# Kernel optimization log

Hardware: AMD Instinct MI355X
Metric: run time of the kernel (lower is better)

## Reference

```python
import jax, jax.numpy as jnp
import numpy as np

B_SZ, L, D_MODEL = 2, 1024, 1024
D_INNER, D_STATE, D_CONV = 2048, 16, 4
EPS = 1e-6


def setup_inputs() -> dict:
    key = jax.random.key(0)
    ks = jax.random.split(key, 8)
    def n(k, shape, scale=0.02):
        return jax.random.normal(k, shape, jnp.float32) * scale
    return {
        "x": jax.random.normal(ks[0], (B_SZ, L, D_MODEL), jnp.float32),
        "W_in": n(ks[1], (D_MODEL, 2 * D_INNER)),
        "b_in": jnp.zeros((2 * D_INNER,), jnp.float32),
        "conv_w": n(ks[2], (D_INNER, 1, D_CONV), 0.2),
        "conv_b": jnp.zeros((D_INNER,), jnp.float32),
        "W_xp": n(ks[3], (D_INNER, 2 * D_STATE)),
        "b_xp": jnp.zeros((2 * D_STATE,), jnp.float32),
        "W_dt": n(ks[4], (D_INNER, D_INNER)),
        "b_dt": jnp.full((D_INNER,), -1.0, jnp.float32),
        # torch code does log(randn) (NaN-prone); use log of positive uniform instead
        "A_log": jnp.log(jax.random.uniform(ks[5], (D_INNER, D_STATE), jnp.float32, 0.5, 1.5)),
        "D_skip": jnp.ones((D_INNER,), jnp.float32),
        "W_out": n(ks[6], (D_INNER, D_MODEL)),
        "b_out": jnp.zeros((D_MODEL,), jnp.float32),
        "alpha": jnp.ones((D_MODEL,), jnp.float32),
        "beta": jnp.zeros((D_MODEL,), jnp.float32),
    }


def _selective_scan(xc, delta, A, Bm, Cm, D_skip):
    # xc, delta: (B,L,di); A: (di,ds); Bm, Cm: (B,L,ds)
    dA = jnp.exp(delta[..., None] * A)                     # (B,L,di,ds)
    dBx = (delta * xc)[..., None] * Bm[:, :, None, :]      # (B,L,di,ds)
    h0 = jnp.zeros((xc.shape[0], xc.shape[2], A.shape[1]), xc.dtype)

    def step(h, inp):
        dA_t, dBx_t, C_t = inp
        h = dA_t * h + dBx_t                               # (B,di,ds)
        y_t = jnp.einsum('bds,bs->bd', h, C_t)
        return h, y_t

    _, ys = jax.lax.scan(
        step, h0,
        (dA.transpose(1, 0, 2, 3), dBx.transpose(1, 0, 2, 3), Cm.transpose(1, 0, 2)))
    y = ys.transpose(1, 0, 2)                              # (B,L,di)
    return y + D_skip * xc


def _layernorm(r, alpha, beta):
    # torch LayerNormalization: unbiased std, eps added to std
    mean = jnp.mean(r, axis=-1, keepdims=True)
    diff = r - mean
    var_unb = jnp.sum(diff * diff, axis=-1, keepdims=True) / (r.shape[-1] - 1)
    std = jnp.sqrt(var_unb)
    return alpha * diff / (std + EPS) + beta


def reference(x, W_in, b_in, conv_w, conv_b, W_xp, b_xp, W_dt, b_dt,
              A_log, D_skip, W_out, b_out, alpha, beta):
    residual = x
    xz = x @ W_in + b_in                                   # (B,L,2*di)
    x_in, z = jnp.split(xz, 2, axis=-1)

    # depthwise causal conv1d (torch pads d_conv-1 both sides, slices [:L])
    xt = x_in.transpose(0, 2, 1)                           # (B,di,L)
    xt = jax.lax.conv_general_dilated(
        xt, conv_w, window_strides=(1,), padding=[(D_CONV - 1, 0)],
        feature_group_count=D_INNER, dimension_numbers=('NCH', 'OIH', 'NCH'))
    xt = xt + conv_b[None, :, None]
    x_conv = jax.nn.silu(xt.transpose(0, 2, 1))            # (B,L,di)

    x_proj_out = x_conv @ W_xp + b_xp                      # (B,L,2*ds)
    Bm, Cm = jnp.split(x_proj_out, 2, axis=-1)
    delta = jax.nn.softplus(x_conv @ W_dt + b_dt)          # (B,L,di)
    A = -jnp.exp(A_log)

    y = _selective_scan(x_conv, delta, A, Bm, Cm, D_skip)
    y = y * jax.nn.silu(z)
    out = y @ W_out + b_out                                # (B,L,D)
    return _layernorm(residual + out, alpha, beta)
```

## Files before the change

kernel.cpp:

```cpp
#include <hip/hip_runtime.h>
#include <math.h>

#define B_SZ    2
#define L_SEQ   1024
#define DMODEL  1024
#define DINNER  2048
#define DSTATE  16
#define EPSV    1e-6f

#define CCH 128
#define CS  (L_SEQ / CCH)
#define DT  8
#define SSTR2 (CCH * DT + 2)

typedef short  bf16x8  __attribute__((ext_vector_type(8)));
typedef float  floatx4 __attribute__((ext_vector_type(4)));
typedef unsigned short ushort8v __attribute__((ext_vector_type(8)));

extern "C" __device__ float __ocml_native_exp2_f32(float);
extern "C" __device__ float __ocml_native_log2_f32(float);

__device__ __forceinline__ float nexp2(float x) { return __ocml_native_exp2_f32(x); }

__device__ __forceinline__ float softplus_f(float v) {
    if (v > 20.f) return v;
    return 0.69314718f * __ocml_native_log2_f32(1.f + nexp2(v * 1.44269504f));
}
__device__ __forceinline__ float silu_f(float z) {
    return z / (1.f + nexp2(z * -1.44269504f));
}

__device__ __forceinline__ unsigned short f2bf(float f) {
    unsigned int u = __float_as_uint(f);
    unsigned int r = (u + 0x7FFFu + ((u >> 16) & 1u)) >> 16;
    return (unsigned short)r;
}
__device__ __forceinline__ float bf2f(unsigned short u) {
    return __uint_as_float(((unsigned int)u) << 16);
}

__global__ __launch_bounds__(256) void prep_kernel(
    const float* __restrict__ x, unsigned short* __restrict__ x_bf,
    const float* __restrict__ W_in, unsigned short* __restrict__ W_in_t,
    const float* __restrict__ W_dt, unsigned short* __restrict__ W_dt_t,
    const float* __restrict__ W_out, unsigned short* __restrict__ W_out_t)
{
    const int bid = blockIdx.x;
    if (bid >= 10240) {
        const int i = (bid - 10240) * 256 + threadIdx.x;
        float4 v = ((const float4*)x)[i];
        ushort4 o = { f2bf(v.x), f2bf(v.y), f2bf(v.z), f2bf(v.w) };
        ((ushort4*)x_bf)[i] = o;
        return;
    }
    __shared__ float tile[32][33];
    const float* W; unsigned short* Wt; int K, N, t;
    if (bid < 4096)      { W = W_in;  Wt = W_in_t;  K = 1024; N = 4096; t = bid; }
    else if (bid < 8192) { W = W_dt;  Wt = W_dt_t;  K = 2048; N = 2048; t = bid - 4096; }
    else                 { W = W_out; Wt = W_out_t; K = 2048; N = 1024; t = bid - 8192; }
    const int nx = N >> 5;
    const int n0 = (t % nx) * 32;
    const int k0 = (t / nx) * 32;
    const int c = threadIdx.x & 31;
    const int r = threadIdx.x >> 5;
#pragma unroll
    for (int i = 0; i < 4; ++i)
        tile[r + 8 * i][c] = W[(size_t)(k0 + r + 8 * i) * N + n0 + c];
    __syncthreads();
#pragma unroll
    for (int i = 0; i < 4; ++i)
        Wt[(size_t)(n0 + r + 8 * i) * K + k0 + c] = f2bf(tile[c][r + 8 * i]);
}

template <int TM, int TN, int MODE, int MINW>
__global__ __launch_bounds__(256, MINW) void gemm_bf16(
    const unsigned short* __restrict__ A, const unsigned short* __restrict__ Bt,
    const float* __restrict__ bias, const float* __restrict__ resid,
    float* __restrict__ C, unsigned short* __restrict__ zout,
    int M, int N, int K)
{
    constexpr int MI = TM / 32;
    constexpr int NJ = TN / 32;
    constexpr int NLOAD = (TM + TN) / 32;

    __shared__ unsigned short As[TM * 64];
    __shared__ unsigned short Bs[TN * 64];

    const int tid  = threadIdx.x;
    const int wave = tid >> 6;
    const int lane = tid & 63;
    const int m0 = blockIdx.y * TM;
    const int n0 = blockIdx.x * TN;
    const int wm = (wave >> 1) * (TM / 2);
    const int wn = (wave & 1) * (TN / 2);
    const int fr = lane & 15;
    const int kg = lane >> 4;

    int offs[NLOAD];
    unsigned short* lp[NLOAD];
#pragma unroll
    for (int i = 0; i < NLOAD; ++i) {
        const int slot = i * 256 + tid;
        const int row  = slot >> 3;
        const int ch   = slot & 7;
        const int pos  = ch ^ (row & 7);
        if (i < TM / 32) {
            offs[i] = (m0 + row) * K + ch * 8;
            lp[i]   = &As[row * 64 + pos * 8];
        } else {
            const int rb = row - TM;
            offs[i] = (n0 + rb) * K + ch * 8;
            lp[i]   = &Bs[rb * 64 + pos * 8];
        }
    }

    floatx4 acc[MI][NJ] = {};
    bf16x8 pre[NLOAD];

#pragma unroll
    for (int i = 0; i < NLOAD; ++i)
        pre[i] = *(const bf16x8*)((i < TM / 32 ? A : Bt) + offs[i]);
#pragma unroll
    for (int i = 0; i < NLOAD; ++i)
        *(bf16x8*)lp[i] = pre[i];
    __syncthreads();

    for (int kt = 0; kt < K; kt += 64) {
        const bool more = (kt + 64) < K;
        if (more) {
#pragma unroll
            for (int i = 0; i < NLOAD; ++i)
                pre[i] = *(const bf16x8*)((i < TM / 32 ? A : Bt) + offs[i] + kt + 64);
        }

#pragma unroll
        for (int ks = 0; ks < 2; ++ks) {
            const int cq = (ks << 2) | kg;
            bf16x8 af[MI], bfv[NJ];
#pragma unroll
            for (int i = 0; i < MI; ++i) {
                const int row = wm + i * 16 + fr;
                af[i] = *(const bf16x8*)&As[row * 64 + ((cq ^ (row & 7)) << 3)];
            }
#pragma unroll
            for (int j = 0; j < NJ; ++j) {
                const int row = wn + j * 16 + fr;
                bfv[j] = *(const bf16x8*)&Bs[row * 64 + ((cq ^ (row & 7)) << 3)];
            }
#pragma unroll
            for (int i = 0; i < MI; ++i)
#pragma unroll
                for (int j = 0; j < NJ; ++j)
                    acc[i][j] = __builtin_amdgcn_mfma_f32_16x16x32_bf16(
                        af[i], bfv[j], acc[i][j], 0, 0, 0);
        }
        __syncthreads();
        if (more) {
#pragma unroll
            for (int i = 0; i < NLOAD; ++i)
                *(bf16x8*)lp[i] = pre[i];
        }
        __syncthreads();
    }

    const int rq = (lane >> 4) * 4;
    if (MODE == 4) {
        unsigned short* Ct = (unsigned short*)C;
#pragma unroll
        for (int i = 0; i < MI; ++i) {
#pragma unroll
            for (int j = 0; j < NJ; ++j) {
                const int col = n0 + wn + j * 16 + fr;
                const float bv = bias[col];
                const int row0 = m0 + wm + i * 16 + rq;
                ushort4 o;
#pragma unroll
                for (int r = 0; r < 4; ++r)
                    (&o.x)[r] = f2bf(softplus_f(acc[i][j][r] + bv));
                *(ushort4*)&Ct[(size_t)col * M + row0] = o;
            }
        }
    } else if (MODE == 5) {
        if (n0 < DINNER) {
#pragma unroll
            for (int i = 0; i < MI; ++i) {
#pragma unroll
                for (int j = 0; j < NJ; ++j) {
                    const int col = n0 + wn + j * 16 + fr;
                    const float bv = bias[col];
#pragma unroll
                    for (int r = 0; r < 4; ++r) {
                        const int row = m0 + wm + i * 16 + rq + r;
                        C[(size_t)row * DINNER + col] = acc[i][j][r] + bv;
                    }
                }
            }
        } else {
#pragma unroll
            for (int i = 0; i < MI; ++i) {
#pragma unroll
                for (int j = 0; j < NJ; ++j) {
                    const int col = n0 + wn + j * 16 + fr;
                    const float bv = bias[col];
                    const int row0 = m0 + wm + i * 16 + rq;
                    ushort4 o;
#pragma unroll
                    for (int r = 0; r < 4; ++r)
                        (&o.x)[r] = f2bf(silu_f(acc[i][j][r] + bv));
                    *(ushort4*)&zout[(size_t)(col - DINNER) * M + row0] = o;
                }
            }
        }
    } else {
#pragma unroll
        for (int i = 0; i < MI; ++i) {
#pragma unroll
            for (int j = 0; j < NJ; ++j) {
                const int col = n0 + wn + j * 16 + fr;
                const float bv = bias[col];
#pragma unroll
                for (int r = 0; r < 4; ++r) {
                    const int row = m0 + wm + i * 16 + rq + r;
                    float v = acc[i][j][r] + bv;
                    if (MODE == 1) {
                        v = softplus_f(v);
                    } else if (MODE == 2) {
                        v += resid[(size_t)row * N + col];
                    }
                    C[(size_t)row * N + col] = v;
                }
            }
        }
    }
}

#define CROWS 4
__global__ __launch_bounds__(256) void conv_xproj(
    const float* __restrict__ x_in, const float* __restrict__ conv_w,
    const float* __restrict__ conv_b, const float* __restrict__ W_xp,
    const float* __restrict__ b_xp,
    unsigned short* __restrict__ x_conv_bf, float* __restrict__ BC)
{
    __shared__ float sxc[CROWS][DINNER];
    __shared__ float red[8][CROWS][32];

    const int tid = threadIdx.x;
    const int r0 = blockIdx.x * CROWS;
    const int c8 = tid * 8;

    float wt[8][4];
#pragma unroll
    for (int ci = 0; ci < 8; ++ci) {
        float4 w4 = *(const float4*)&conv_w[(c8 + ci) * 4];
        wt[ci][0] = w4.x; wt[ci][1] = w4.y; wt[ci][2] = w4.z; wt[ci][3] = w4.w;
    }
    float cb[8];
    *(float4*)&cb[0] = *(const float4*)&conv_b[c8];
    *(float4*)&cb[4] = *(const float4*)&conv_b[c8 + 4];

#pragma unroll
    for (int rr = 0; rr < CROWS; ++rr) {
        const int row = r0 + rr;
        const int l = row & (L_SEQ - 1);
        float acc[8];
#pragma unroll
        for (int ci = 0; ci < 8; ++ci) acc[ci] = cb[ci];
#pragma unroll
        for (int h = 0; h < 4; ++h) {
            const int lsrc = l - 3 + h;
            if (lsrc >= 0) {
                float4 a = *(const float4*)&x_in[(size_t)(row - 3 + h) * DINNER + c8];
                float4 b = *(const float4*)&x_in[(size_t)(row - 3 + h) * DINNER + c8 + 4];
                acc[0] += a.x * wt[0][h]; acc[1] += a.y * wt[1][h];
                acc[2] += a.z * wt[2][h]; acc[3] += a.w * wt[3][h];
                acc[4] += b.x * wt[4][h]; acc[5] += b.y * wt[5][h];
                acc[6] += b.z * wt[6][h]; acc[7] += b.w * wt[7][h];
            }
        }
        float o[8];
        ushort8v ob;
#pragma unroll
        for (int ci = 0; ci < 8; ++ci) {
            o[ci] = silu_f(acc[ci]);
            sxc[rr][c8 + ci] = o[ci];
            ob[ci] = (short)f2bf(o[ci]);
        }
        *(ushort8v*)&x_conv_bf[(size_t)row * DINNER + c8] = ob;
    }
    __syncthreads();

    const int n = tid & 31;
    const int g = tid >> 5;
    float p[CROWS] = {};
    const int k0 = g * 256;
#pragma unroll 4
    for (int k = k0; k < k0 + 256; ++k) {
        const float wv = W_xp[k * 32 + n];
        p[0] += sxc[0][k] * wv;
        p[1] += sxc[1][k] * wv;
        p[2] += sxc[2][k] * wv;
        p[3] += sxc[3][k] * wv;
    }
#pragma unroll
    for (int rr = 0; rr < CROWS; ++rr) red[g][rr][n] = p[rr];
    __syncthreads();
    if (tid < CROWS * 32) {
        const int rr = tid >> 5;
        const int n2 = tid & 31;
        float s = b_xp[n2];
#pragma unroll
        for (int gg = 0; gg < 8; ++gg) s += red[gg][rr][n2];
        BC[(size_t)(r0 + rr) * 32 + n2] = s;
    }
}

__global__ __launch_bounds__(1024, 4) void scan_kernel(
    const unsigned short* __restrict__ deltaT,
    const unsigned short* __restrict__ xc_bf,
    const float* __restrict__ BC, const float* __restrict__ A_log,
    const float* __restrict__ D_skip, const unsigned short* __restrict__ zt,
    unsigned short* __restrict__ y_bf)
{
    __shared__ unsigned short sA[DSTATE * SSTR2];
    __shared__ unsigned short sH[DSTATE * SSTR2];

    const int tid = threadIdx.x;
    const int dl  = tid & (DT - 1);
    const int c   = tid >> 3;
    const int b   = blockIdx.x >> 8;
    const int d0  = (blockIdx.x & 255) * DT;
    const int d   = d0 + dl;

    float Al[DSTATE];
#pragma unroll
    for (int s = 0; s < DSTATE; ++s)
        Al[s] = -__expf(A_log[d * DSTATE + s]) * 1.44269504f;
    const float Dsk = D_skip[d];

    const int l0 = c * CS;
    const int row0 = b * L_SEQ + l0;

    const unsigned short* dpt = deltaT + (size_t)d * (B_SZ * L_SEQ) + row0;
    bf16x8 dv0 = *(const bf16x8*)dpt;
    const unsigned short* gpt = zt + (size_t)d * (B_SZ * L_SEQ) + row0;
    bf16x8 gv0 = *(const bf16x8*)gpt;

    float dts[CS];
    float dsum = 0.f;
#pragma unroll
    for (int k = 0; k < CS; ++k) {
        dts[k] = bf2f((unsigned short)dv0[k]);
        dsum += dts[k];
    }

    float h[DSTATE];
#pragma unroll
    for (int s = 0; s < DSTATE; ++s) h[s] = 0.f;

    const unsigned short* xcp = xc_bf + (size_t)row0 * DINNER + d;
    const float* bcp = BC + (size_t)row0 * 32;

#pragma unroll 4
    for (int j = 0; j < CS; ++j) {
        const float dt = dts[j];
        const float xc = bf2f(xcp[j * DINNER]);
        float Bv[DSTATE];
        *(float4*)&Bv[0]  = *(const float4*)(bcp + j * 32 + 0);
        *(float4*)&Bv[4]  = *(const float4*)(bcp + j * 32 + 4);
        *(float4*)&Bv[8]  = *(const float4*)(bcp + j * 32 + 8);
        *(float4*)&Bv[12] = *(const float4*)(bcp + j * 32 + 12);
        const float dlx = dt * xc;
#pragma unroll
        for (int s = 0; s < DSTATE; ++s) {
            const float e = nexp2(dt * Al[s]);
            h[s] = e * h[s] + dlx * Bv[s];
        }
    }
#pragma unroll
    for (int s = 0; s < DSTATE; ++s) {
        sH[s * SSTR2 + tid] = f2bf(h[s]);
        sA[s * SSTR2 + tid] = f2bf(nexp2(Al[s] * dsum));
    }
    __syncthreads();

    if (tid < DSTATE * DT) {
        const int dl2 = tid & (DT - 1);
        const int s2  = tid >> 3;
        float hh = 0.f;
        for (int c2 = 0; c2 < CCH; ++c2) {
            const int idx = s2 * SSTR2 + c2 * DT + dl2;
            const float a  = bf2f(sA[idx]);
            const float he = bf2f(sH[idx]);
            sH[idx] = f2bf(hh);
            hh = a * hh + he;
        }
    }
    __syncthreads();

#pragma unroll
    for (int s = 0; s < DSTATE; ++s) h[s] = bf2f(sH[s * SSTR2 + tid]);

    unsigned short* yp = y_bf + (size_t)row0 * DINNER + d;
#pragma unroll
    for (int j = 0; j < CS; ++j) {
        const float dt = dts[j];
        const float xc = bf2f(xcp[j * DINNER]);
        const float g  = bf2f((unsigned short)gv0[j]);
        float Bv[DSTATE], Cv[DSTATE];
        *(float4*)&Bv[0]  = *(const float4*)(bcp + j * 32 + 0);
        *(float4*)&Bv[4]  = *(const float4*)(bcp + j * 32 + 4);
        *(float4*)&Bv[8]  = *(const float4*)(bcp + j * 32 + 8);
        *(float4*)&Bv[12] = *(const float4*)(bcp + j * 32 + 12);
        *(float4*)&Cv[0]  = *(const float4*)(bcp + j * 32 + 16);
        *(float4*)&Cv[4]  = *(const float4*)(bcp + j * 32 + 20);
        *(float4*)&Cv[8]  = *(const float4*)(bcp + j * 32 + 24);
        *(float4*)&Cv[12] = *(const float4*)(bcp + j * 32 + 28);
        const float dlx = dt * xc;
        float y = Dsk * xc;
#pragma unroll
        for (int s = 0; s < DSTATE; ++s) {
            const float e = nexp2(dt * Al[s]);
            h[s] = e * h[s] + dlx * Bv[s];
            y += h[s] * Cv[s];
        }
        yp[j * DINNER] = f2bf(y * g);
    }
}

__global__ __launch_bounds__(256) void layernorm_kernel(
    const float* __restrict__ t, const float* __restrict__ alpha,
    const float* __restrict__ beta, float* __restrict__ out)
{
    __shared__ float sred[4];
    __shared__ float sred2[4];
    const int row = blockIdx.x;
    const int tid = threadIdx.x;
    const float* r = t + (size_t)row * DMODEL;

    float4 v = *(const float4*)&r[tid * 4];
    float lsum = v.x + v.y + v.z + v.w;
#pragma unroll
    for (int m = 1; m < 64; m <<= 1) lsum += __shfl_xor(lsum, m);
    if ((tid & 63) == 0) sred[tid >> 6] = lsum;
    __syncthreads();
    const float mean = (sred[0] + sred[1] + sred[2] + sred[3]) * (1.f / DMODEL);

    const float dx = v.x - mean, dy = v.y - mean, dz = v.z - mean, dw = v.w - mean;
    float ls2 = dx * dx + dy * dy + dz * dz + dw * dw;
#pragma unroll
    for (int m = 1; m < 64; m <<= 1) ls2 += __shfl_xor(ls2, m);
    if ((tid & 63) == 0) sred2[tid >> 6] = ls2;
    __syncthreads();
    const float var = (sred2[0] + sred2[1] + sred2[2] + sred2[3]) * (1.f / (DMODEL - 1));
    const float inv = 1.f / (sqrtf(var) + EPSV);

    float4 a4 = *(const float4*)&alpha[tid * 4];
    float4 b4 = *(const float4*)&beta[tid * 4];
    float4 o;
    o.x = a4.x * dx * inv + b4.x;
    o.y = a4.y * dy * inv + b4.y;
    o.z = a4.z * dz * inv + b4.z;
    o.w = a4.w * dw * inv + b4.w;
    *(float4*)&out[(size_t)row * DMODEL + tid * 4] = o;
}

extern "C" void kernel_launch(void* const* d_in, const int* in_sizes, int n_in,
                              void* d_out, int out_size, void* d_ws, size_t ws_size,
                              hipStream_t stream)
{
    const float* x      = (const float*)d_in[0];
    const float* W_in   = (const float*)d_in[1];
    const float* b_in   = (const float*)d_in[2];
    const float* conv_w = (const float*)d_in[3];
    const float* conv_b = (const float*)d_in[4];
    const float* W_xp   = (const float*)d_in[5];
    const float* b_xp   = (const float*)d_in[6];
    const float* W_dt   = (const float*)d_in[7];
    const float* b_dt   = (const float*)d_in[8];
    const float* A_log  = (const float*)d_in[9];
    const float* D_skip = (const float*)d_in[10];
    const float* W_out  = (const float*)d_in[11];
    const float* b_out  = (const float*)d_in[12];
    const float* alpha  = (const float*)d_in[13];
    const float* beta   = (const float*)d_in[14];
    float* out = (float*)d_out;

    const size_t M = (size_t)B_SZ * L_SEQ;
    char* ws = (char*)d_ws;
    float* x_in    = (float*)(ws + 0);
    unsigned short* zt = (unsigned short*)(ws + (16u << 20));
    unsigned short* deltaT = (unsigned short*)(ws + (48u << 20));
    float* BC      = (float*)(ws + (64u << 20));
    unsigned short* x_bf       = (unsigned short*)(ws + (64u << 20) + (512u << 10));
    unsigned short* W_in_t     = (unsigned short*)(ws + (69u << 20));
    unsigned short* W_dt_t     = (unsigned short*)(ws + (77u << 20));
    unsigned short* W_out_t    = (unsigned short*)(ws + (85u << 20));
    unsigned short* x_conv_bf  = (unsigned short*)(ws + (89u << 20));
    unsigned short* ygate_bf   = (unsigned short*)(ws + (77u << 20));
    float* tpre = x_in;

    const dim3 blk(256);

    prep_kernel<<<dim3(12288), blk, 0, stream>>>(
        x, x_bf, W_in, W_in_t, W_dt, W_dt_t, W_out, W_out_t);

    gemm_bf16<128, 128, 5, 2><<<dim3(4096 / 128, 2048 / 128), blk, 0, stream>>>(
        x_bf, W_in_t, b_in, nullptr, x_in, zt, 2048, 4096, 1024);

    conv_xproj<<<dim3((unsigned)(M / CROWS)), blk, 0, stream>>>(
        x_in, conv_w, conv_b, W_xp, b_xp, x_conv_bf, BC);

    gemm_bf16<128, 64, 4, 3><<<dim3(2048 / 64, 2048 / 128), blk, 0, stream>>>(
        x_conv_bf, W_dt_t, b_dt, nullptr, (float*)deltaT, nullptr, 2048, 2048, 2048);

    scan_kernel<<<dim3(B_SZ * (DINNER / DT)), dim3(1024), 0, stream>>>(
        deltaT, x_conv_bf, BC, A_log, D_skip, zt, ygate_bf);

    gemm_bf16<64, 64, 2, 3><<<dim3(1024 / 64, 2048 / 64), blk, 0, stream>>>(
        ygate_bf, W_out_t, b_out, x, tpre, nullptr, 2048, 1024, 2048);

    layernorm_kernel<<<dim3((unsigned)M), blk, 0, stream>>>(tpre, alpha, beta, out);
}
```

Before: 277.4 us.

## Pre-transpose x_conv for scan and compute chunk decay from shared dsum

Adds a bf16 transpose kernel that writes x_conv in (d, row) layout, so each scan thread loads its 8 timesteps as one vector load. This replaces 8 strided scalar loads, each a DINNER stride apart. The scan's shared sA array is replaced by a float per-thread dsum array, and the chunk-carry threads recompute exp2(A*dsum) on the fly. This cuts shared memory and keeps the decay factor in fp32. The cost is an extra kernel launch plus a 8MB read/write pass, and the workspace region at offset 24MB must not overlap zt, which is still in use.

Result: no change. 272.9 us (-1.6%).

```diff
diff --git a/kernel.cpp b/kernel.cpp
--- a/kernel.cpp
+++ b/kernel.cpp
@@ -11,7 +11,7 @@
 #define CCH 128
 #define CS  (L_SEQ / CCH)
 #define DT  8
-#define SSTR2 (CCH * DT + 2)
+#define SSTR 1032
 
 typedef short  bf16x8  __attribute__((ext_vector_type(8)));
 typedef float  floatx4 __attribute__((ext_vector_type(4)));
@@ -70,6 +70,33 @@
 #pragma unroll
     for (int i = 0; i < 4; ++i)
         Wt[(size_t)(n0 + r + 8 * i) * K + k0 + c] = f2bf(tile[c][r + 8 * i]);
+}
+
+__global__ __launch_bounds__(256) void transp_bf16(
+    const unsigned short* __restrict__ in, unsigned short* __restrict__ outp)
+{
+    __shared__ unsigned short tile[64][66];
+    const int bx = blockIdx.x & 31;
+    const int by = blockIdx.x >> 5;
+    const int m0 = bx * 64, d0 = by * 64;
+    const int tid = threadIdx.x;
+    const int r = tid >> 3;
+    const int c = (tid & 7) * 8;
+#pragma unroll
+    for (int i = 0; i < 2; ++i) {
+        const int row = r + i * 32;
+        ushort8v v = *(const ushort8v*)&in[(size_t)(m0 + row) * DINNER + d0 + c];
+        *(ushort8v*)&tile[row][c] = v;
+    }
+    __syncthreads();
+#pragma unroll
+    for (int i = 0; i < 2; ++i) {
+        const int dd = r + i * 32;
+        ushort8v o;
+#pragma unroll
+        for (int k = 0; k < 8; ++k) o[k] = tile[c + k][dd];
+        *(ushort8v*)&outp[(size_t)(d0 + dd) * (B_SZ * L_SEQ) + m0 + c] = o;
+    }
 }
 
 template <int TM, int TN, int MODE, int MINW>
@@ -316,13 +343,13 @@
 
 __global__ __launch_bounds__(1024, 4) void scan_kernel(
     const unsigned short* __restrict__ deltaT,
-    const unsigned short* __restrict__ xc_bf,
+    const unsigned short* __restrict__ xcT,
     const float* __restrict__ BC, const float* __restrict__ A_log,
     const float* __restrict__ D_skip, const unsigned short* __restrict__ zt,
     unsigned short* __restrict__ y_bf)
 {
-    __shared__ unsigned short sA[DSTATE * SSTR2];
-    __shared__ unsigned short sH[DSTATE * SSTR2];
+    __shared__ unsigned short sH[DSTATE * SSTR];
+    __shared__ float sDsum[CCH * DT];
 
     const int tid = threadIdx.x;
     const int dl  = tid & (DT - 1);
@@ -331,25 +358,28 @@
     const int d0  = (blockIdx.x & 255) * DT;
     const int d   = d0 + dl;
 
+    const int l0 = c * CS;
+    const int row0 = b * L_SEQ + l0;
+
+    const unsigned short* dpt = deltaT + (size_t)d * (B_SZ * L_SEQ) + row0;
+    bf16x8 dv0 = *(const bf16x8*)dpt;
+    const unsigned short* xpt = xcT + (size_t)d * (B_SZ * L_SEQ) + row0;
+    bf16x8 xv0 = *(const bf16x8*)xpt;
+    const unsigned short* gpt = zt + (size_t)d * (B_SZ * L_SEQ) + row0;
+    bf16x8 gv0 = *(const bf16x8*)gpt;
+
     float Al[DSTATE];
 #pragma unroll
     for (int s = 0; s < DSTATE; ++s)
         Al[s] = -__expf(A_log[d * DSTATE + s]) * 1.44269504f;
     const float Dsk = D_skip[d];
 
-    const int l0 = c * CS;
-    const int row0 = b * L_SEQ + l0;
-
-    const unsigned short* dpt = deltaT + (size_t)d * (B_SZ * L_SEQ) + row0;
-    bf16x8 dv0 = *(const bf16x8*)dpt;
-    const unsigned short* gpt = zt + (size_t)d * (B_SZ * L_SEQ) + row0;
-    bf16x8 gv0 = *(const bf16x8*)gpt;
-
-    float dts[CS];
+    float dts[CS], xcs[CS];
     float dsum = 0.f;
 #pragma unroll
     for (int k = 0; k < CS; ++k) {
         dts[k] = bf2f((unsigned short)dv0[k]);
+        xcs[k] = bf2f((unsigned short)xv0[k]);
         dsum += dts[k];
     }
 
@@ -357,13 +387,12 @@
 #pragma unroll
     for (int s = 0; s < DSTATE; ++s) h[s] = 0.f;
 
-    const unsigned short* xcp = xc_bf + (size_t)row0 * DINNER + d;
     const float* bcp = BC + (size_t)row0 * 32;
 
 #pragma unroll 4
     for (int j = 0; j < CS; ++j) {
         const float dt = dts[j];
-        const float xc = bf2f(xcp[j * DINNER]);
+        const float xc = xcs[j];
         float Bv[DSTATE];
         *(float4*)&Bv[0]  = *(const float4*)(bcp + j * 32 + 0);
         *(float4*)&Bv[4]  = *(const float4*)(bcp + j * 32 + 4);
@@ -377,19 +406,19 @@
         }
     }
 #pragma unroll
-    for (int s = 0; s < DSTATE; ++s) {
-        sH[s * SSTR2 + tid] = f2bf(h[s]);
-        sA[s * SSTR2 + tid] = f2bf(nexp2(Al[s] * dsum));
-    }
+    for (int s = 0; s < DSTATE; ++s)
+        sH[s * SSTR + tid] = f2bf(h[s]);
+    sDsum[tid] = dsum;
     __syncthreads();
 
     if (tid < DSTATE * DT) {
         const int dl2 = tid & (DT - 1);
         const int s2  = tid >> 3;
+        const float Alc = -__expf(A_log[(d0 + dl2) * DSTATE + s2]) * 1.44269504f;
         float hh = 0.f;
         for (int c2 = 0; c2 < CCH; ++c2) {
-            const int idx = s2 * SSTR2 + c2 * DT + dl2;
-            const float a  = bf2f(sA[idx]);
+            const int idx = s2 * SSTR + c2 * DT + dl2;
+            const float a  = nexp2(Alc * sDsum[c2 * DT + dl2]);
             const float he = bf2f(sH[idx]);
             sH[idx] = f2bf(hh);
             hh = a * hh + he;
@@ -398,13 +427,13 @@
     __syncthreads();
 
 #pragma unroll
-    for (int s = 0; s < DSTATE; ++s) h[s] = bf2f(sH[s * SSTR2 + tid]);
+    for (int s = 0; s < DSTATE; ++s) h[s] = bf2f(sH[s * SSTR + tid]);
 
     unsigned short* yp = y_bf + (size_t)row0 * DINNER + d;
 #pragma unroll
     for (int j = 0; j < CS; ++j) {
         const float dt = dts[j];
-        const float xc = bf2f(xcp[j * DINNER]);
+        const float xc = xcs[j];
         const float g  = bf2f((unsigned short)gv0[j]);
         float Bv[DSTATE], Cv[DSTATE];
         *(float4*)&Bv[0]  = *(const float4*)(bcp + j * 32 + 0);
@@ -496,6 +525,7 @@
     unsigned short* W_dt_t     = (unsigned short*)(ws + (77u << 20));
     unsigned short* W_out_t    = (unsigned short*)(ws + (85u << 20));
     unsigned short* x_conv_bf  = (unsigned short*)(ws + (89u << 20));
+    unsigned short* xcT        = (unsigned short*)(ws + (24u << 20));
     unsigned short* ygate_bf   = (unsigned short*)(ws + (77u << 20));
     float* tpre = x_in;
 
@@ -510,11 +540,13 @@
     conv_xproj<<<dim3((unsigned)(M / CROWS)), blk, 0, stream>>>(
         x_in, conv_w, conv_b, W_xp, b_xp, x_conv_bf, BC);
 
+    transp_bf16<<<dim3(1024), blk, 0, stream>>>(x_conv_bf, xcT);
+
     gemm_bf16<128, 64, 4, 3><<<dim3(2048 / 64, 2048 / 128), blk, 0, stream>>>(
         x_conv_bf, W_dt_t, b_dt, nullptr, (float*)deltaT, nullptr, 2048, 2048, 2048);
 
     scan_kernel<<<dim3(B_SZ * (DINNER / DT)), dim3(1024), 0, stream>>>(
-        deltaT, x_conv_bf, BC, A_log, D_skip, zt, ygate_bf);
+        deltaT, xcT, BC, A_log, D_skip, zt, ygate_bf);
 
     gemm_bf16<64, 64, 2, 3><<<dim3(1024 / 64, 2048 / 64), blk, 0, stream>>>(
         ygate_bf, W_out_t, b_out, x, tpre, nullptr, 2048, 1024, 2048);
```
